# Kernel tuning notes

Hardware: AMD Instinct MI355X
Metric: run time of the kernel (lower is better)

The kernel has to match this reference:

```python
import jax, jax.numpy as jnp
import numpy as np

N_EMBD = 768
N_HEAD = 12
HEAD_DIM = N_EMBD // N_HEAD


def setup_inputs() -> dict:
    key = jax.random.key(0)
    k1, k2, k3 = jax.random.split(key, 3)
    B, T, C = 4, 2048, N_EMBD
    x = jax.random.normal(k1, (B, T, C), dtype=jnp.float32)
    # c_attn: torch Linear(C, 3C) -> store as (C, 3C) for x @ W
    w_attn = jax.random.normal(k2, (C, 3 * C), dtype=jnp.float32) * (1.0 / np.sqrt(C))
    b_attn = jax.random.normal(k3, (3 * C,), dtype=jnp.float32) * 0.02
    return {"x": x, "w_attn": w_attn, "b_attn": b_attn}


def reference(x, w_attn, b_attn):
    B, T, C = x.shape
    H, D = N_HEAD, HEAD_DIM
    scale = 1.0 / np.sqrt(D).astype(np.float32)

    qkv = x @ w_attn + b_attn                      # (B, T, 3C)
    q, k, v = jnp.split(qkv, 3, axis=-1)
    q = q.reshape(B, T, H, D).transpose(0, 2, 1, 3)  # (B, H, T, D)
    k = k.reshape(B, T, H, D).transpose(0, 2, 1, 3)
    v = v.reshape(B, T, H, D).transpose(0, 2, 1, 3)

    att = jnp.einsum('bhid,bhjd->bhij', q, k) * scale  # (B, H, T, T)
    causal = jnp.tril(jnp.ones((T, T), dtype=bool))
    # masked positions -> -inf -> relu -> 0; kept positions -> relu(scaled score)
    att = jnp.where(causal, jnp.maximum(att, 0.0), 0.0)

    y = jnp.einsum('bhij,bhjd->bhid', att, v)      # (B, H, T, D)
    y = y.transpose(0, 2, 1, 3).reshape(B, T, C)
    return y
```

## Files before the change

kernel.cpp:

```cpp
#include <hip/hip_runtime.h>
#include <hip/hip_bf16.h>

typedef short bf16x8 __attribute__((ext_vector_type(8)));
typedef float f32x4  __attribute__((ext_vector_type(4)));
typedef unsigned short u16x4 __attribute__((ext_vector_type(4)));

#define CDIM   768
#define NQKV   2304
#define MROWS  8192
#define TSEQ   2048
#define HD     64
#define NHEAD  12
#define BHTOT  48

__device__ __forceinline__ unsigned short f2bf(float f) {
    unsigned int x;
    __builtin_memcpy(&x, &f, 4);
    unsigned int r = (x + 0x7fffu + ((x >> 16) & 1u)) >> 16;
    return (unsigned short)r;
}

__device__ __forceinline__ unsigned int pkbf(float a, float b) {
    unsigned int ua, ub;
    __builtin_memcpy(&ua, &a, 4);
    __builtin_memcpy(&ub, &b, 4);
    return __builtin_amdgcn_perm(ua + 0x8000u, ub + 0x8000u, 0x03020706u);
}

__device__ __forceinline__ f32x4 mfma16(bf16x8 a, bf16x8 b, f32x4 c) {
    return __builtin_amdgcn_mfma_f32_16x16x32_bf16(a, b, c, 0, 0, 0);
}

__device__ __forceinline__ void gl_lds16(const unsigned short* g, unsigned short* l) {
    __builtin_amdgcn_global_load_lds(
        (__attribute__((address_space(1))) void*)(g),
        (__attribute__((address_space(3))) void*)(l),
        16, 0, 0);
}

__global__ __launch_bounds__(256) void prep(
    const float* __restrict__ X, const float* __restrict__ W,
    unsigned short* __restrict__ Xb, unsigned short* __restrict__ Wt)
{
    const int tid = threadIdx.x, blk = blockIdx.x;
    if (blk < 432) {
        __shared__ __align__(16) unsigned short tile[64][72];
        const int bx = blk % 36, by = blk / 36;
#pragma unroll
        for (int c = 0; c < 4; c++) {
            int chunk = tid + 256 * c;
            int r = chunk >> 4, cc = chunk & 15;
            f32x4 v = *(const f32x4*)(W + (size_t)(by * 64 + r) * NQKV + bx * 64 + cc * 4);
#pragma unroll
            for (int j = 0; j < 4; j++) tile[cc * 4 + j][r] = f2bf(v[j]);
        }
        __syncthreads();
#pragma unroll
        for (int c = 0; c < 2; c++) {
            int chunk = tid + 256 * c;
            int r = chunk >> 3, cc = chunk & 7;
            bf16x8 v;
#pragma unroll
            for (int j = 0; j < 8; j++) v[j] = (short)tile[r][cc * 8 + j];
            *(bf16x8*)(Wt + (size_t)(bx * 64 + r) * CDIM + by * 64 + cc * 8) = v;
        }
    }
    for (size_t i4 = (size_t)blk * 256 + tid; i4 < (size_t)(MROWS * CDIM / 4);
         i4 += (size_t)448 * 256) {
        f32x4 v = *(const f32x4*)(X + i4 * 4);
        u16x4 o;
#pragma unroll
        for (int j = 0; j < 4; j++) o[j] = f2bf(v[j]);
        *(u16x4*)(Xb + i4 * 4) = o;
    }
}

#define BK 64

__global__ __launch_bounds__(512, 4) void qkv_gemm(
    const unsigned short* __restrict__ X,
    const unsigned short* __restrict__ Wt,
    const float* __restrict__ Bias,
    unsigned short* __restrict__ Q,
    unsigned short* __restrict__ Km,
    unsigned short* __restrict__ Vt)
{
    __shared__ __align__(16) unsigned short As[256 * BK];
    __shared__ __align__(16) unsigned short Bs[128 * BK];
    const int tid  = threadIdx.x;
    const int wave = tid >> 6, lane = tid & 63;
    const int quad = lane >> 4, m16 = lane & 15;
    const int wr = wave >> 1, wc = wave & 1;

    const int t   = blockIdx.x;
    const int xcd = t & 7, s = t >> 3;
    const int m0  = (xcd * 4 + (s & 3)) * 256;
    const int n0  = (s >> 2) * 128;

    f32x4 acc[4][4];
#pragma unroll
    for (int i = 0; i < 4; i++)
#pragma unroll
        for (int j = 0; j < 4; j++) acc[i][j] = f32x4{0.f, 0.f, 0.f, 0.f};

    const unsigned short* xb = X + (size_t)m0 * CDIM;
    const unsigned short* wb = Wt + (size_t)n0 * CDIM;

    const int spos = lane & 7;
    const int rb = m16 & 7;
    int arow[4], brow[2];
#pragma unroll
    for (int c = 0; c < 4; c++) arow[c] = (wave * 256 + c * 64 + lane) >> 3;
#pragma unroll
    for (int c = 0; c < 2; c++) brow[c] = (wave * 128 + c * 64 + lane) >> 3;

    for (int k0 = 0; k0 < CDIM; k0 += BK) {
#pragma unroll
        for (int c = 0; c < 4; c++) {
            int row = arow[c], ch = spos ^ (row & 7);
            gl_lds16(xb + (size_t)row * CDIM + k0 + ch * 8, As + wave * 2048 + c * 512);
        }
#pragma unroll
        for (int c = 0; c < 2; c++) {
            int row = brow[c], ch = spos ^ (row & 7);
            gl_lds16(wb + (size_t)row * CDIM + k0 + ch * 8, Bs + wave * 1024 + c * 512);
        }
        __syncthreads();
#pragma unroll
        for (int ks = 0; ks < 2; ks++) {
            bf16x8 af[4], bfg[4];
#pragma unroll
            for (int u = 0; u < 4; u++) {
                int rowa = wr * 64 + u * 16 + m16;
                int rowb = wc * 64 + u * 16 + m16;
                int pos = (ks * 4 + quad) ^ rb;
                af[u]  = *(const bf16x8*)(As + rowa * 64 + pos * 8);
                bfg[u] = *(const bf16x8*)(Bs + rowb * 64 + pos * 8);
            }
#pragma unroll
            for (int i = 0; i < 4; i++)
#pragma unroll
                for (int j = 0; j < 4; j++)
                    acc[i][j] = mfma16(af[i], bfg[j], acc[i][j]);
        }
        __syncthreads();
    }

    const int region = n0 / CDIM;
    const float qscale = (region == 0) ? 0.125f : 1.0f;
#pragma unroll
    for (int i = 0; i < 4; i++) {
        int row = m0 + wr * 64 + i * 16 + quad * 4;
#pragma unroll
        for (int j = 0; j < 4; j++) {
            int gcol = n0 + wc * 64 + j * 16 + m16;
            int cc = gcol - region * CDIM;
            int h = cc >> 6, d = cc & 63;
            float bv = Bias[gcol];
#pragma unroll
            for (int r = 0; r < 4; r++) {
                int gm = row + r;
                int b = gm >> 11, tq = gm & 2047;
                int bh = b * NHEAD + h;
                unsigned short o = f2bf((acc[i][j][r] + bv) * qscale);
                if (region == 0)      Q[((size_t)bh * TSEQ + tq) * HD + d] = o;
                else if (region == 1) Km[((size_t)bh * TSEQ + tq) * HD + d] = o;
                else                  Vt[((size_t)bh * HD + d) * TSEQ + tq] = o;
            }
        }
    }
}

#define LDSK 0
#define LDSV 8192

__global__ __launch_bounds__(256, 4) void attn(
    const unsigned short* __restrict__ Q,
    const unsigned short* __restrict__ Kmat,
    const unsigned short* __restrict__ Vt,
    float* __restrict__ Out)
{
    __shared__ __align__(16) unsigned short S[16384];

    const int tid  = threadIdx.x;
    const int wave = tid >> 6, lane = tid & 63;
    const int q4 = lane >> 4, m16 = lane & 15;
    const int q8 = m16 >> 2, m3 = m16 & 3;

    const int xcd = blockIdx.x & 7;
    const int idx = blockIdx.x >> 3;
    const int bh  = xcd * 6 + (idx % 6);
    const int it  = 15 - (idx / 6);
    const int i0  = it * 128;

    const unsigned short* qb = Q    + (size_t)bh * TSEQ * HD;
    const unsigned short* kb = Kmat + (size_t)bh * TSEQ * HD;
    const unsigned short* vb = Vt   + (size_t)bh * HD * TSEQ;

    bf16x8 qf[2][2];
#pragma unroll
    for (int si = 0; si < 2; si++)
#pragma unroll
        for (int ks = 0; ks < 2; ks++)
            qf[si][ks] = *(const bf16x8*)(qb +
                (size_t)(i0 + wave * 32 + si * 16 + m16) * HD + ks * 32 + q4 * 8);

    f32x4 oacc[2][4];
#pragma unroll
    for (int si = 0; si < 2; si++)
#pragma unroll
        for (int dn = 0; dn < 4; dn++) oacc[si][dn] = f32x4{0.f, 0.f, 0.f, 0.f};

    const int fr  = ((q8 & 1) << 2) | m3;
    const int kx0 = (q4 ^ fr) * 8;
    const int kx1 = kx0 ^ 32;
    const int krb = (q8 * 8 + m3) * 64;

    for (int jt = 0; jt <= it; jt++) {
        const int j0 = jt * 128;
#pragma unroll
        for (int cc = 0; cc < 4; cc++) {
            int cs = wave * 4 + cc;
            {
                int rowK = cs * 8 + (lane >> 3);
                int chK  = (lane & 7) ^ ((((rowK >> 3) & 1) << 2) | (rowK & 3));
                gl_lds16(kb + (size_t)(j0 + rowK) * HD + chK * 8, &S[LDSK] + cs * 512);
            }
            {
                int dV  = cs * 4 + (lane >> 4);
                int chV = (m16 & 8) | ((m16 ^ dV) & 7);
                gl_lds16(vb + (size_t)dV * TSEQ + j0 + chV * 8, &S[LDSV] + cs * 512);
            }
        }
        __syncthreads();

        const bool diag = (jt == it);
#pragma unroll
        for (int kk = 0; kk < 4; kk++) {
            const int kb0 = kk * 2048 + krb;
            bf16x8 kf_e0 = *(const bf16x8*)(&S[LDSK] + kb0 + kx0);
            bf16x8 kf_e1 = *(const bf16x8*)(&S[LDSK] + kb0 + kx1);
            bf16x8 kf_o0 = *(const bf16x8*)(&S[LDSK] + kb0 + 256 + kx0);
            bf16x8 kf_o1 = *(const bf16x8*)(&S[LDSK] + kb0 + 256 + kx1);

            f32x4 sacc[2][2];
#pragma unroll
            for (int o = 0; o < 2; o++)
#pragma unroll
                for (int si = 0; si < 2; si++) sacc[o][si] = f32x4{0.f, 0.f, 0.f, 0.f};
#pragma unroll
            for (int si = 0; si < 2; si++) {
                sacc[0][si] = mfma16(kf_e0, qf[si][0], sacc[0][si]);
                sacc[0][si] = mfma16(kf_e1, qf[si][1], sacc[0][si]);
                sacc[1][si] = mfma16(kf_o0, qf[si][0], sacc[1][si]);
                sacc[1][si] = mfma16(kf_o1, qf[si][1], sacc[1][si]);
            }

            unsigned int pk[2][2][2];
#pragma unroll
            for (int o = 0; o < 2; o++)
#pragma unroll
                for (int si = 0; si < 2; si++) {
                    f32x4 v = sacc[o][si];
                    if (diag) {
#pragma unroll
                        for (int r = 0; r < 4; r++) {
                            int gj = kk * 32 + q4 * 8 + o * 4 + r;
                            int gi = wave * 32 + si * 16 + m16;
                            if (gj > gi) v[r] = 0.f;
                        }
                    }
#pragma unroll
                    for (int r = 0; r < 4; r++) v[r] = fmaxf(v[r], 0.f);
                    pk[o][si][0] = pkbf(v[0], v[1]);
                    pk[o][si][1] = pkbf(v[2], v[3]);
                }

#pragma unroll
            for (int dn = 0; dn < 4; dn++) {
                int vsw = ((kk * 4 + q4) ^ (m16 & 7)) * 8;
                bf16x8 vf = *(const bf16x8*)(&S[LDSV] + (dn * 16 + m16) * 128 + vsw);
#pragma unroll
                for (int si = 0; si < 2; si++) {
                    union { bf16x8 v; unsigned int u[4]; } af;
                    af.u[0] = pk[0][si][0];
                    af.u[1] = pk[0][si][1];
                    af.u[2] = pk[1][si][0];
                    af.u[3] = pk[1][si][1];
                    oacc[si][dn] = mfma16(af.v, vf, oacc[si][dn]);
                }
            }
        }
        __syncthreads();
    }

    const int b = bh / NHEAD, h = bh % NHEAD;
#pragma unroll
    for (int si = 0; si < 2; si++) {
        int ri = i0 + wave * 32 + si * 16 + q4 * 4;
#pragma unroll
        for (int dn = 0; dn < 4; dn++) {
            int d = dn * 16 + m16;
#pragma unroll
            for (int r = 0; r < 4; r++) {
                Out[((size_t)b * TSEQ + ri + r) * CDIM + h * HD + d] = oacc[si][dn][r];
            }
        }
    }
}

extern "C" void kernel_launch(void* const* d_in, const int* in_sizes, int n_in,
                              void* d_out, int out_size, void* d_ws, size_t ws_size,
                              hipStream_t stream) {
    const float* X    = (const float*)d_in[0];
    const float* W    = (const float*)d_in[1];
    const float* Bias = (const float*)d_in[2];
    float* out = (float*)d_out;

    unsigned short* Xb = (unsigned short*)d_ws;
    unsigned short* Wt = Xb + (size_t)MROWS * CDIM;
    unsigned short* Q  = Wt + (size_t)NQKV * CDIM;
    unsigned short* Km = Q  + (size_t)BHTOT * TSEQ * HD;
    unsigned short* Vt = Km + (size_t)BHTOT * TSEQ * HD;

    hipLaunchKernelGGL(prep, dim3(448), dim3(256), 0, stream, X, W, Xb, Wt);
    hipLaunchKernelGGL(qkv_gemm, dim3(576), dim3(512), 0, stream,
                       Xb, Wt, Bias, Q, Km, Vt);
    hipLaunchKernelGGL(attn, dim3(BHTOT * 16), dim3(256), 0, stream, Q, Km, Vt, out);
}
```

Before: 180.2 us.

## Triple-buffer QKV GEMM K-loop with async global-to-LDS prefetch and split barriers

Replaces the single-buffered QKV GEMM main loop with a three-stage LDS ring. Tiles two steps ahead are issued as global-to-LDS loads while the current tile is computed, with the A and B loads interleaved between two MFMA half-steps. It uses explicit vmcnt/lgkmcnt waits, s_barrier and setprio, and precomputes global and LDS offsets. The goal is to hide global load latency behind MFMA work. In exchange, LDS use triples and launch bounds drop to 2 blocks per CU, which lowers occupancy.

```diff
diff --git a/kernel.cpp b/kernel.cpp
--- a/kernel.cpp
+++ b/kernel.cpp
@@ -76,8 +76,9 @@
 }
 
 #define BK 64
-
-__global__ __launch_bounds__(512, 4) void qkv_gemm(
+#define NTILES 12
+
+__global__ __launch_bounds__(512, 2) void qkv_gemm(
     const unsigned short* __restrict__ X,
     const unsigned short* __restrict__ Wt,
     const float* __restrict__ Bias,
@@ -85,8 +86,8 @@
     unsigned short* __restrict__ Km,
     unsigned short* __restrict__ Vt)
 {
-    __shared__ __align__(16) unsigned short As[256 * BK];
-    __shared__ __align__(16) unsigned short Bs[128 * BK];
+    __shared__ __align__(16) unsigned short As[3 * 256 * BK];
+    __shared__ __align__(16) unsigned short Bs[3 * 128 * BK];
     const int tid  = threadIdx.x;
     const int wave = tid >> 6, lane = tid & 63;
     const int quad = lane >> 4, m16 = lane & 15;
@@ -107,43 +108,107 @@
     const unsigned short* wb = Wt + (size_t)n0 * CDIM;
 
     const int spos = lane & 7;
-    const int rb = m16 & 7;
-    int arow[4], brow[2];
-#pragma unroll
-    for (int c = 0; c < 4; c++) arow[c] = (wave * 256 + c * 64 + lane) >> 3;
-#pragma unroll
-    for (int c = 0; c < 2; c++) brow[c] = (wave * 128 + c * 64 + lane) >> 3;
-
-    for (int k0 = 0; k0 < CDIM; k0 += BK) {
-#pragma unroll
-        for (int c = 0; c < 4; c++) {
-            int row = arow[c], ch = spos ^ (row & 7);
-            gl_lds16(xb + (size_t)row * CDIM + k0 + ch * 8, As + wave * 2048 + c * 512);
-        }
-#pragma unroll
-        for (int c = 0; c < 2; c++) {
-            int row = brow[c], ch = spos ^ (row & 7);
-            gl_lds16(wb + (size_t)row * CDIM + k0 + ch * 8, Bs + wave * 1024 + c * 512);
-        }
-        __syncthreads();
-#pragma unroll
-        for (int ks = 0; ks < 2; ks++) {
-            bf16x8 af[4], bfg[4];
-#pragma unroll
-            for (int u = 0; u < 4; u++) {
-                int rowa = wr * 64 + u * 16 + m16;
-                int rowb = wc * 64 + u * 16 + m16;
-                int pos = (ks * 4 + quad) ^ rb;
-                af[u]  = *(const bf16x8*)(As + rowa * 64 + pos * 8);
-                bfg[u] = *(const bf16x8*)(Bs + rowb * 64 + pos * 8);
-            }
-#pragma unroll
-            for (int i = 0; i < 4; i++)
-#pragma unroll
-                for (int j = 0; j < 4; j++)
-                    acc[i][j] = mfma16(af[i], bfg[j], acc[i][j]);
-        }
-        __syncthreads();
+    const int rb   = m16 & 7;
+
+    size_t agoff[4];
+    size_t bgoff[2];
+#pragma unroll
+    for (int c = 0; c < 4; c++) {
+        int row = (wave * 256 + c * 64 + lane) >> 3;
+        agoff[c] = (size_t)row * CDIM + (spos ^ (row & 7)) * 8;
+    }
+#pragma unroll
+    for (int c = 0; c < 2; c++) {
+        int row = (wave * 128 + c * 64 + lane) >> 3;
+        bgoff[c] = (size_t)row * CDIM + (spos ^ (row & 7)) * 8;
+    }
+    unsigned short* aDst = As + wave * 2048;
+    unsigned short* bDst = Bs + wave * 1024;
+
+    const int posk0 = (quad ^ rb) * 8;
+    const int posk1 = ((4 + quad) ^ rb) * 8;
+    int arof[4], brof[4];
+#pragma unroll
+    for (int u = 0; u < 4; u++) arof[u] = (wr * 64 + u * 16 + m16) * 64;
+#pragma unroll
+    for (int j = 0; j < 4; j++) brof[j] = (wc * 64 + j * 16 + m16) * 64;
+
+    gl_lds16(xb + agoff[0], aDst);
+    gl_lds16(xb + agoff[1], aDst + 512);
+    gl_lds16(xb + agoff[2], aDst + 1024);
+    gl_lds16(xb + agoff[3], aDst + 1536);
+    gl_lds16(wb + bgoff[0], bDst);
+    gl_lds16(wb + bgoff[1], bDst + 512);
+    gl_lds16(xb + agoff[0] + 64, aDst + 16384);
+    gl_lds16(xb + agoff[1] + 64, aDst + 16384 + 512);
+    gl_lds16(xb + agoff[2] + 64, aDst + 16384 + 1024);
+    gl_lds16(xb + agoff[3] + 64, aDst + 16384 + 1536);
+    gl_lds16(wb + bgoff[0] + 64, bDst + 8192);
+    gl_lds16(wb + bgoff[1] + 64, bDst + 8192 + 512);
+    asm volatile("s_waitcnt vmcnt(6)" ::: "memory");
+    __builtin_amdgcn_s_barrier();
+
+    int qb = 0, qn = 2;
+#pragma unroll 1
+    for (int tt = 0; tt < NTILES; ++tt) {
+        const unsigned short* Aq = As + qb * 16384;
+        const unsigned short* Bq = Bs + qb * 8192;
+        const int kn = (tt + 2) * 64;
+        const bool st = (tt < NTILES - 2);
+
+        bf16x8 a0[4], bA[4];
+#pragma unroll
+        for (int u = 0; u < 4; u++)
+            a0[u] = *(const bf16x8*)(Aq + arof[u] + posk0);
+#pragma unroll
+        for (int j = 0; j < 4; j++)
+            bA[j] = *(const bf16x8*)(Bq + brof[j] + posk0);
+        if (st) {
+            gl_lds16(xb + agoff[0] + kn, aDst + qn * 16384);
+            gl_lds16(xb + agoff[1] + kn, aDst + qn * 16384 + 512);
+            gl_lds16(xb + agoff[2] + kn, aDst + qn * 16384 + 1024);
+            gl_lds16(xb + agoff[3] + kn, aDst + qn * 16384 + 1536);
+        }
+        __builtin_amdgcn_s_barrier();
+        asm volatile("s_waitcnt lgkmcnt(0)" ::: "memory");
+        __builtin_amdgcn_s_setprio(1);
+#pragma unroll
+        for (int i = 0; i < 4; i++)
+#pragma unroll
+            for (int j = 0; j < 4; j++)
+                acc[i][j] = mfma16(a0[i], bA[j], acc[i][j]);
+        __builtin_amdgcn_s_setprio(0);
+        __builtin_amdgcn_s_barrier();
+
+        bf16x8 a1[4], bB[4];
+#pragma unroll
+        for (int u = 0; u < 4; u++)
+            a1[u] = *(const bf16x8*)(Aq + arof[u] + posk1);
+#pragma unroll
+        for (int j = 0; j < 4; j++)
+            bB[j] = *(const bf16x8*)(Bq + brof[j] + posk1);
+        if (st) {
+            gl_lds16(wb + bgoff[0] + kn, bDst + qn * 8192);
+            gl_lds16(wb + bgoff[1] + kn, bDst + qn * 8192 + 512);
+        }
+        if (tt < NTILES - 2) {
+            asm volatile("s_waitcnt vmcnt(6)" ::: "memory");
+        } else if (tt == NTILES - 2) {
+            asm volatile("s_waitcnt vmcnt(0)" ::: "memory");
+        }
+        __builtin_amdgcn_s_barrier();
+        asm volatile("s_waitcnt lgkmcnt(0)" ::: "memory");
+        __builtin_amdgcn_s_setprio(1);
+#pragma unroll
+        for (int i = 0; i < 4; i++)
+#pragma unroll
+            for (int j = 0; j < 4; j++)
+                acc[i][j] = mfma16(a1[i], bB[j], acc[i][j]);
+        __builtin_amdgcn_s_setprio(0);
+        __builtin_amdgcn_s_barrier();
+
+        qb = (qb == 2) ? 0 : qb + 1;
+        qn = (qn == 2) ? 0 : qn + 1;
     }
 
     const int region = n0 / CDIM;
```

Result: no change. 183.7 us (+2.0%).

## Double-buffer QKV GEMM LDS tiles with BK=32 and overlap loads with MFMA

Applied to the files above, without the earlier changes.

Switches the QKV projection GEMM from a single-buffered BK=64 loop, which synchronised twice per step, to a ping-pong double buffer with BK=32. The next tile is issued via global-to-LDS loads before computing on the current one, leaving one barrier per half-step. It also precomputes swizzled LDS offsets and raises wave priority around the MFMA blocks. The goal is to hide global load latency behind matrix math, at the cost of more iterations and barriers from the smaller K tile.

```diff
diff --git a/kernel.cpp b/kernel.cpp
--- a/kernel.cpp
+++ b/kernel.cpp
@@ -75,7 +75,8 @@
     }
 }
 
-#define BK 64
+#define BK 32
+#define NT 24
 
 __global__ __launch_bounds__(512, 4) void qkv_gemm(
     const unsigned short* __restrict__ X,
@@ -85,8 +86,8 @@
     unsigned short* __restrict__ Km,
     unsigned short* __restrict__ Vt)
 {
-    __shared__ __align__(16) unsigned short As[256 * BK];
-    __shared__ __align__(16) unsigned short Bs[128 * BK];
+    __shared__ __align__(16) unsigned short As[2 * 256 * BK];
+    __shared__ __align__(16) unsigned short Bs[2 * 128 * BK];
     const int tid  = threadIdx.x;
     const int wave = tid >> 6, lane = tid & 63;
     const int quad = lane >> 4, m16 = lane & 15;
@@ -106,44 +107,88 @@
     const unsigned short* xb = X + (size_t)m0 * CDIM;
     const unsigned short* wb = Wt + (size_t)n0 * CDIM;
 
-    const int spos = lane & 7;
-    const int rb = m16 & 7;
-    int arow[4], brow[2];
-#pragma unroll
-    for (int c = 0; c < 4; c++) arow[c] = (wave * 256 + c * 64 + lane) >> 3;
-#pragma unroll
-    for (int c = 0; c < 2; c++) brow[c] = (wave * 128 + c * 64 + lane) >> 3;
-
-    for (int k0 = 0; k0 < CDIM; k0 += BK) {
-#pragma unroll
-        for (int c = 0; c < 4; c++) {
-            int row = arow[c], ch = spos ^ (row & 7);
-            gl_lds16(xb + (size_t)row * CDIM + k0 + ch * 8, As + wave * 2048 + c * 512);
-        }
-#pragma unroll
-        for (int c = 0; c < 2; c++) {
-            int row = brow[c], ch = spos ^ (row & 7);
-            gl_lds16(wb + (size_t)row * CDIM + k0 + ch * 8, Bs + wave * 1024 + c * 512);
-        }
-        __syncthreads();
-#pragma unroll
-        for (int ks = 0; ks < 2; ks++) {
+    const unsigned short* xa0;
+    const unsigned short* xa1;
+    const unsigned short* wbp;
+    {
+        int id0 = tid;
+        int id1 = 512 + tid;
+        int r0 = id0 >> 2, cl0 = id0 & 3, cg0 = cl0 ^ ((r0 >> 1) & 3);
+        int r1 = id1 >> 2, cl1 = id1 & 3, cg1 = cl1 ^ ((r1 >> 1) & 3);
+        xa0 = xb + (size_t)r0 * CDIM + cg0 * 8;
+        xa1 = xb + (size_t)r1 * CDIM + cg1 * 8;
+        int rb = tid >> 2, clb = tid & 3, cgb = clb ^ ((rb >> 1) & 3);
+        wbp = wb + (size_t)rb * CDIM + cgb * 8;
+    }
+    const int dA0 = wave * 512;
+    const int dA1 = 4096 + wave * 512;
+    const int dB  = wave * 512;
+
+    int aro[4], bro[4];
+#pragma unroll
+    for (int u = 0; u < 4; u++) {
+        int r = wr * 64 + u * 16 + m16;
+        aro[u] = r * 32 + (quad ^ ((r >> 1) & 3)) * 8;
+    }
+#pragma unroll
+    for (int j = 0; j < 4; j++) {
+        int r = wc * 64 + j * 16 + m16;
+        bro[j] = r * 32 + (quad ^ ((r >> 1) & 3)) * 8;
+    }
+
+    gl_lds16(xa0, As + dA0);
+    gl_lds16(xa1, As + dA1);
+    gl_lds16(wbp, Bs + dB);
+    asm volatile("s_waitcnt vmcnt(0)" ::: "memory");
+    __builtin_amdgcn_s_barrier();
+
+#pragma unroll 1
+    for (int tt = 0; tt < NT; tt += 2) {
+        {
+            const int kk = (tt + 1) * BK;
+            gl_lds16(xa0 + kk, As + 8192 + dA0);
+            gl_lds16(xa1 + kk, As + 8192 + dA1);
+            gl_lds16(wbp + kk, Bs + 4096 + dB);
             bf16x8 af[4], bfg[4];
 #pragma unroll
-            for (int u = 0; u < 4; u++) {
-                int rowa = wr * 64 + u * 16 + m16;
-                int rowb = wc * 64 + u * 16 + m16;
-                int pos = (ks * 4 + quad) ^ rb;
-                af[u]  = *(const bf16x8*)(As + rowa * 64 + pos * 8);
-                bfg[u] = *(const bf16x8*)(Bs + rowb * 64 + pos * 8);
-            }
+            for (int u = 0; u < 4; u++) af[u]  = *(const bf16x8*)(As + aro[u]);
+#pragma unroll
+            for (int j = 0; j < 4; j++) bfg[j] = *(const bf16x8*)(Bs + bro[j]);
+            __builtin_amdgcn_s_setprio(1);
 #pragma unroll
             for (int i = 0; i < 4; i++)
 #pragma unroll
                 for (int j = 0; j < 4; j++)
                     acc[i][j] = mfma16(af[i], bfg[j], acc[i][j]);
-        }
-        __syncthreads();
+            __builtin_amdgcn_s_setprio(0);
+            asm volatile("s_waitcnt vmcnt(0)" ::: "memory");
+            __builtin_amdgcn_s_barrier();
+        }
+        {
+            const bool st = (tt + 2 < NT);
+            if (st) {
+                const int kk = (tt + 2) * BK;
+                gl_lds16(xa0 + kk, As + dA0);
+                gl_lds16(xa1 + kk, As + dA1);
+                gl_lds16(wbp + kk, Bs + dB);
+            }
+            bf16x8 af[4], bfg[4];
+#pragma unroll
+            for (int u = 0; u < 4; u++) af[u]  = *(const bf16x8*)(As + 8192 + aro[u]);
+#pragma unroll
+            for (int j = 0; j < 4; j++) bfg[j] = *(const bf16x8*)(Bs + 4096 + bro[j]);
+            __builtin_amdgcn_s_setprio(1);
+#pragma unroll
+            for (int i = 0; i < 4; i++)
+#pragma unroll
+                for (int j = 0; j < 4; j++)
+                    acc[i][j] = mfma16(af[i], bfg[j], acc[i][j]);
+            __builtin_amdgcn_s_setprio(0);
+            if (st) {
+                asm volatile("s_waitcnt vmcnt(0)" ::: "memory");
+                __builtin_amdgcn_s_barrier();
+            }
+        }
     }
 
     const int region = n0 / CDIM;
```

Result: no change. 183.2 us (+1.7%).

## Double-buffer QKV GEMM with 256x256 tiles and prefetch of the next K slab

Applied to the files above, without the earlier changes.

The QKV projection GEMM moves from 256x128 tiles to 256x256 tiles, halving the grid to 288 blocks. Each block gets a 128 KB LDS double buffer so the next K slab is loaded asynchronously while MFMAs run on the current one, replacing two barriers per step with one. MFMA sections are wrapped in s_setprio, and blocks are remapped with an XCD-aware swizzle. The aim is to hide global-load latency and raise operand reuse, at the cost of more accumulator registers and lower occupancy (launch bounds drop to 2), with 288 blocks on 256 CUs leaving a partial second wave.

```diff
diff --git a/kernel.cpp b/kernel.cpp
--- a/kernel.cpp
+++ b/kernel.cpp
@@ -75,9 +75,9 @@
     }
 }
 
-#define BK 64
-
-__global__ __launch_bounds__(512, 4) void qkv_gemm(
+#define QKV_NT 12
+
+__global__ __launch_bounds__(512, 2) void qkv_gemm(
     const unsigned short* __restrict__ X,
     const unsigned short* __restrict__ Wt,
     const float* __restrict__ Bias,
@@ -85,75 +85,110 @@
     unsigned short* __restrict__ Km,
     unsigned short* __restrict__ Vt)
 {
-    __shared__ __align__(16) unsigned short As[256 * BK];
-    __shared__ __align__(16) unsigned short Bs[128 * BK];
+    __shared__ __align__(16) unsigned short S[65536];
+
     const int tid  = threadIdx.x;
     const int wave = tid >> 6, lane = tid & 63;
     const int quad = lane >> 4, m16 = lane & 15;
-    const int wr = wave >> 1, wc = wave & 1;
-
-    const int t   = blockIdx.x;
-    const int xcd = t & 7, s = t >> 3;
-    const int m0  = (xcd * 4 + (s & 3)) * 256;
-    const int n0  = (s >> 2) * 128;
-
-    f32x4 acc[4][4];
-#pragma unroll
-    for (int i = 0; i < 4; i++)
-#pragma unroll
-        for (int j = 0; j < 4; j++) acc[i][j] = f32x4{0.f, 0.f, 0.f, 0.f};
-
-    const unsigned short* xb = X + (size_t)m0 * CDIM;
+    const int wm = wave >> 2, wn = wave & 3;
+
+    const int swz = (blockIdx.x & 7) * 36 + (blockIdx.x >> 3);
+    const int mt = swz & 31, nt = swz >> 5;
+    const int m0 = mt * 256, n0 = nt * 256;
+
+    f32x4 acc[8][4];
+#pragma unroll
+    for (int u = 0; u < 8; u++)
+#pragma unroll
+        for (int j = 0; j < 4; j++) acc[u][j] = f32x4{0.f, 0.f, 0.f, 0.f};
+
+    const unsigned short* xb = X  + (size_t)m0 * CDIM;
     const unsigned short* wb = Wt + (size_t)n0 * CDIM;
 
-    const int spos = lane & 7;
-    const int rb = m16 & 7;
-    int arow[4], brow[2];
-#pragma unroll
-    for (int c = 0; c < 4; c++) arow[c] = (wave * 256 + c * 64 + lane) >> 3;
-#pragma unroll
-    for (int c = 0; c < 2; c++) brow[c] = (wave * 128 + c * 64 + lane) >> 3;
-
-    for (int k0 = 0; k0 < CDIM; k0 += BK) {
-#pragma unroll
-        for (int c = 0; c < 4; c++) {
-            int row = arow[c], ch = spos ^ (row & 7);
-            gl_lds16(xb + (size_t)row * CDIM + k0 + ch * 8, As + wave * 2048 + c * 512);
-        }
-#pragma unroll
-        for (int c = 0; c < 2; c++) {
-            int row = brow[c], ch = spos ^ (row & 7);
-            gl_lds16(wb + (size_t)row * CDIM + k0 + ch * 8, Bs + wave * 1024 + c * 512);
-        }
-        __syncthreads();
-#pragma unroll
-        for (int ks = 0; ks < 2; ks++) {
-            bf16x8 af[4], bfg[4];
-#pragma unroll
-            for (int u = 0; u < 4; u++) {
-                int rowa = wr * 64 + u * 16 + m16;
-                int rowb = wc * 64 + u * 16 + m16;
-                int pos = (ks * 4 + quad) ^ rb;
-                af[u]  = *(const bf16x8*)(As + rowa * 64 + pos * 8);
-                bfg[u] = *(const bf16x8*)(Bs + rowb * 64 + pos * 8);
-            }
-#pragma unroll
-            for (int i = 0; i < 4; i++)
-#pragma unroll
-                for (int j = 0; j < 4; j++)
-                    acc[i][j] = mfma16(af[i], bfg[j], acc[i][j]);
-        }
-        __syncthreads();
-    }
+    size_t soff[4];
+#pragma unroll
+    for (int c = 0; c < 4; c++) {
+        int ch = wave * 256 + c * 64 + lane;
+        int r  = ch >> 3;
+        int cg = (ch & 7) ^ (r & 7);
+        soff[c] = (size_t)r * CDIM + cg * 8;
+    }
+    const int dstA = wave * 2048;
+    const int dstB = 16384 + wave * 2048;
+
+    int aof[2][8], bof[2][4];
+#pragma unroll
+    for (int u = 0; u < 8; u++) {
+        int r = wm * 128 + u * 16 + m16;
+        aof[0][u] = r * 64 + ((0 * 4 + quad) ^ (r & 7)) * 8;
+        aof[1][u] = r * 64 + ((1 * 4 + quad) ^ (r & 7)) * 8;
+    }
+#pragma unroll
+    for (int j = 0; j < 4; j++) {
+        int r = wn * 64 + j * 16 + m16;
+        bof[0][j] = 16384 + r * 64 + ((0 * 4 + quad) ^ (r & 7)) * 8;
+        bof[1][j] = 16384 + r * 64 + ((1 * 4 + quad) ^ (r & 7)) * 8;
+    }
+
+#pragma unroll
+    for (int c = 0; c < 4; c++) gl_lds16(xb + soff[c], S + dstA + c * 512);
+#pragma unroll
+    for (int c = 0; c < 4; c++) gl_lds16(wb + soff[c], S + dstB + c * 512);
+    asm volatile("s_waitcnt vmcnt(0)" ::: "memory");
+    __builtin_amdgcn_s_barrier();
+
+#define QKV_STEP(CUR, TT)                                                     \
+    {                                                                         \
+        const bool st_ = ((TT) + 1 < QKV_NT);                                 \
+        if (st_) {                                                            \
+            const int kk_ = ((TT) + 1) * 64;                                  \
+            _Pragma("unroll")                                                 \
+            for (int c = 0; c < 4; c++)                                       \
+                gl_lds16(xb + soff[c] + kk_,                                  \
+                         S + ((CUR) ^ 1) * 32768 + dstA + c * 512);           \
+            _Pragma("unroll")                                                 \
+            for (int c = 0; c < 4; c++)                                       \
+                gl_lds16(wb + soff[c] + kk_,                                  \
+                         S + ((CUR) ^ 1) * 32768 + dstB + c * 512);           \
+        }                                                                     \
+        _Pragma("unroll")                                                     \
+        for (int ks = 0; ks < 2; ks++) {                                      \
+            bf16x8 bfr[4], afr[8];                                            \
+            _Pragma("unroll")                                                 \
+            for (int j = 0; j < 4; j++)                                       \
+                bfr[j] = *(const bf16x8*)(S + (CUR) * 32768 + bof[ks][j]);    \
+            _Pragma("unroll")                                                 \
+            for (int u = 0; u < 8; u++)                                       \
+                afr[u] = *(const bf16x8*)(S + (CUR) * 32768 + aof[ks][u]);    \
+            __builtin_amdgcn_s_setprio(1);                                    \
+            _Pragma("unroll")                                                 \
+            for (int u = 0; u < 8; u++)                                       \
+                _Pragma("unroll")                                             \
+                for (int j = 0; j < 4; j++)                                   \
+                    acc[u][j] = mfma16(afr[u], bfr[j], acc[u][j]);            \
+            __builtin_amdgcn_s_setprio(0);                                    \
+        }                                                                     \
+        if (st_) {                                                            \
+            asm volatile("s_waitcnt vmcnt(0)" ::: "memory");                  \
+            __builtin_amdgcn_s_barrier();                                     \
+        }                                                                     \
+    }
+
+#pragma unroll 1
+    for (int tt = 0; tt < QKV_NT; tt += 2) {
+        QKV_STEP(0, tt)
+        QKV_STEP(1, tt + 1)
+    }
+#undef QKV_STEP
 
     const int region = n0 / CDIM;
     const float qscale = (region == 0) ? 0.125f : 1.0f;
 #pragma unroll
-    for (int i = 0; i < 4; i++) {
-        int row = m0 + wr * 64 + i * 16 + quad * 4;
+    for (int u = 0; u < 8; u++) {
+        int row = m0 + wm * 128 + u * 16 + quad * 4;
 #pragma unroll
         for (int j = 0; j < 4; j++) {
-            int gcol = n0 + wc * 64 + j * 16 + m16;
+            int gcol = n0 + wn * 64 + j * 16 + m16;
             int cc = gcol - region * CDIM;
             int h = cc >> 6, d = cc & 63;
             float bv = Bias[gcol];
@@ -162,7 +197,7 @@
                 int gm = row + r;
                 int b = gm >> 11, tq = gm & 2047;
                 int bh = b * NHEAD + h;
-                unsigned short o = f2bf((acc[i][j][r] + bv) * qscale);
+                unsigned short o = f2bf((acc[u][j][r] + bv) * qscale);
                 if (region == 0)      Q[((size_t)bh * TSEQ + tq) * HD + d] = o;
                 else if (region == 1) Km[((size_t)bh * TSEQ + tq) * HD + d] = o;
                 else                  Vt[((size_t)bh * HD + d) * TSEQ + tq] = o;
@@ -324,7 +359,7 @@
     unsigned short* Vt = Km + (size_t)BHTOT * TSEQ * HD;
 
     hipLaunchKernelGGL(prep, dim3(448), dim3(256), 0, stream, X, W, Xb, Wt);
-    hipLaunchKernelGGL(qkv_gemm, dim3(576), dim3(512), 0, stream,
+    hipLaunchKernelGGL(qkv_gemm, dim3(288), dim3(512), 0, stream,
                        Xb, Wt, Bias, Q, Km, Vt);
     hipLaunchKernelGGL(attn, dim3(BHTOT * 16), dim3(256), 0, stream, Q, Km, Vt, out);
 }
```

Measured after the change: 250.6 us. 1.39x slower.
